# Optimization experiments

Hardware: AMD Instinct MI355X
Metric: run time of the kernel (lower is better)

## Reference

```python
import jax, jax.numpy as jnp
import numpy as np

B = 4096            # batch
D = 2048            # inp_dim
H = 16              # head_num
HD = 128            # head_dim; H*HD == D (required by residual + hidden reshape)
NB = H              # BlockLinear num_blocks = head_num
BD = HD // NB       # 8, block size inside each head vector
PROJ = int((4.0 / 3.0) * H * HD)  # 2730
EPS_LN = float(D)   # flax nn.LayerNorm(inp_dim): first positional arg is epsilon (source bug, replicated)
EPS_GN = 1e-6       # flax GroupNorm default epsilon


def setup_inputs() -> dict:
    key = jax.random.key(0)
    ks = jax.random.split(key, 12)
    s = 0.02
    rn = lambda k, shape: (jax.random.normal(k, shape) * s).astype(jnp.float32)
    return {
        'seq': jax.random.normal(ks[0], (B, D), jnp.float32),
        'c_tm1': jnp.zeros((B, H * HD), jnp.float32),
        'n_tm1': jnp.ones((B, H * HD), jnp.float32),
        'h_tm1': jnp.zeros((B, H * HD), jnp.float32),
        'm_tm1': jnp.zeros((B, H * HD), jnp.float32),
        'ln_scale': jnp.ones((D,), jnp.float32),
        'ln_bias': jnp.zeros((D,), jnp.float32),
        'W_z': rn(ks[1], (D, H * HD)), 'b_z': jnp.zeros((H * HD,), jnp.float32),
        'W_i': rn(ks[2], (D, H * HD)), 'b_i': jnp.zeros((H * HD,), jnp.float32),
        'W_f': rn(ks[3], (D, H * HD)), 'b_f': jnp.zeros((H * HD,), jnp.float32),
        'W_o': rn(ks[4], (D, H * HD)), 'b_o': jnp.zeros((H * HD,), jnp.float32),
        'R_z_w': rn(ks[5], (NB, BD, BD)), 'R_z_b': jnp.zeros((NB, BD), jnp.float32),
        'R_i_w': rn(ks[6], (NB, BD, BD)), 'R_i_b': jnp.zeros((NB, BD), jnp.float32),
        'R_f_w': rn(ks[7], (NB, BD, BD)), 'R_f_b': jnp.zeros((NB, BD), jnp.float32),
        'R_o_w': rn(ks[8], (NB, BD, BD)), 'R_o_b': jnp.zeros((NB, BD), jnp.float32),
        'gn_scale': jnp.ones((HD,), jnp.float32),
        'gn_bias': jnp.zeros((HD,), jnp.float32),
        'up_w': rn(ks[9], (H * HD, 2 * PROJ)), 'up_b': jnp.zeros((2 * PROJ,), jnp.float32),
        'down_w': rn(ks[10], (PROJ, D)), 'down_b': jnp.zeros((D,), jnp.float32),
    }


def reference(seq, c_tm1, n_tm1, h_tm1, m_tm1, ln_scale, ln_bias,
              W_z, b_z, W_i, b_i, W_f, b_f, W_o, b_o,
              R_z_w, R_z_b, R_i_w, R_i_b, R_f_w, R_f_b, R_o_w, R_o_b,
              gn_scale, gn_bias, up_w, up_b, down_w, down_b):
    Bq = seq.shape[0]
    # LayerNorm (epsilon == inp_dim, replicating the flax positional-arg quirk)
    mu = jnp.mean(seq, axis=-1, keepdims=True)
    var = jnp.mean((seq - mu) ** 2, axis=-1, keepdims=True)
    x_t = (seq - mu) / jnp.sqrt(var + EPS_LN) * ln_scale + ln_bias
    x_c = x_t  # use_conv=False path

    # Block-diagonal recurrence: h (B,H,HD) -> (B,H,NB,BD), same (BD,BD) block per head
    h_blk = h_tm1.reshape(Bq, H, NB, BD)
    def blk(w, b):
        return (jnp.einsum('bhnd,nde->bhne', h_blk, w) + b).reshape(Bq, -1)

    i_t = x_c @ W_i + b_i + blk(R_i_w, R_i_b)
    f_t = x_c @ W_f + b_f + blk(R_f_w, R_f_b)
    z_t = x_t @ W_z + b_z + blk(R_z_w, R_z_b)
    o_t = x_t @ W_o + b_o + blk(R_o_w, R_o_b)

    # max-stabilized exponential gating
    m_t = jnp.maximum(f_t + m_tm1, i_t)
    i_e = jnp.exp(i_t - m_t)
    f_e = jnp.exp(f_t - m_t + m_tm1)
    z = jnp.tanh(z_t)
    o = jax.nn.sigmoid(o_t)
    c_t = f_e * c_tm1 + i_e * z
    n_t = f_e * n_tm1 + i_e
    h_t = o * (c_t / n_t)

    # flax GroupNorm(num_groups=H) on (B, H, HD): channels=HD split into H groups,
    # reduction over the spatial head axis and each channel group, per (B, group)
    G = H
    Dg = HD // G
    x4 = h_t.reshape(Bq, H, G, Dg)
    mu2 = jnp.mean(x4, axis=(1, 3), keepdims=True)
    var2 = jnp.mean((x4 - mu2) ** 2, axis=(1, 3), keepdims=True)
    xn = ((x4 - mu2) / jnp.sqrt(var2 + EPS_GN)).reshape(Bq, H, HD)
    out = (xn * gn_scale + gn_bias).reshape(Bq, -1)

    up = out @ up_w + up_b
    out1, out2 = jnp.split(up, 2, axis=-1)
    out = (out1 + jax.nn.gelu(out2)) @ down_w + down_b
    return (out + seq, (c_t, n_t, h_t, m_t))
```

## Files before the change

kernel.cpp:

```cpp
#include <hip/hip_runtime.h>
#include <hip/hip_bf16.h>
#include <math.h>

#define BATCH 4096
#define DIM   2048
#define PROJ  2730
#define UPN   5460
#define KPAD  2816
#define NUP   5504
#define NG    8192
#define ROWF  8388608ull

typedef __attribute__((ext_vector_type(8))) short          bf16x8;
typedef __attribute__((ext_vector_type(4))) float          f32x4;
typedef __attribute__((ext_vector_type(8))) unsigned short ushort8;

__device__ __forceinline__ unsigned short f2b(float f) {
    unsigned u = __builtin_bit_cast(unsigned, f);
    u += 0x7fffu + ((u >> 16) & 1u);
    return (unsigned short)(u >> 16);
}
__device__ __forceinline__ float b2f(unsigned short h) {
    unsigned u = ((unsigned)h) << 16;
    return __builtin_bit_cast(float, u);
}

__global__ __launch_bounds__(256)
void ln_kernel(const float* __restrict__ seq, const float* __restrict__ sc,
               const float* __restrict__ bi, unsigned short* __restrict__ X)
{
    __shared__ float red[4][2];
    int b = blockIdx.x, tid = threadIdx.x;
    const float* row = seq + (size_t)b * DIM;
    float4 v0 = ((const float4*)row)[tid];
    float4 v1 = ((const float4*)row)[tid + 256];
    float s  = v0.x + v0.y + v0.z + v0.w + v1.x + v1.y + v1.z + v1.w;
    float ss = v0.x*v0.x + v0.y*v0.y + v0.z*v0.z + v0.w*v0.w
             + v1.x*v1.x + v1.y*v1.y + v1.z*v1.z + v1.w*v1.w;
    #pragma unroll
    for (int off = 32; off; off >>= 1) { s += __shfl_down(s, off); ss += __shfl_down(ss, off); }
    int wid = tid >> 6, lane = tid & 63;
    if (lane == 0) { red[wid][0] = s; red[wid][1] = ss; }
    __syncthreads();
    if (tid == 0) {
        float S = 0.f, SS = 0.f;
        #pragma unroll
        for (int w = 0; w < 4; ++w) { S += red[w][0]; SS += red[w][1]; }
        float mu  = S * (1.0f / DIM);
        float var = SS * (1.0f / DIM) - mu * mu;
        red[0][0] = mu;
        red[0][1] = rsqrtf(var + 2048.0f);
    }
    __syncthreads();
    float mu = red[0][0], r = red[0][1];
    unsigned short* xr = X + (size_t)b * DIM;
    {
        float4 s0 = ((const float4*)sc)[tid];
        float4 b0 = ((const float4*)bi)[tid];
        ushort4 o;
        o.x = f2b((v0.x - mu) * r * s0.x + b0.x);
        o.y = f2b((v0.y - mu) * r * s0.y + b0.y);
        o.z = f2b((v0.z - mu) * r * s0.z + b0.z);
        o.w = f2b((v0.w - mu) * r * s0.w + b0.w);
        ((ushort4*)xr)[tid] = o;
    }
    {
        float4 s1 = ((const float4*)sc)[tid + 256];
        float4 b1 = ((const float4*)bi)[tid + 256];
        ushort4 o;
        o.x = f2b((v1.x - mu) * r * s1.x + b1.x);
        o.y = f2b((v1.y - mu) * r * s1.y + b1.y);
        o.z = f2b((v1.z - mu) * r * s1.z + b1.z);
        o.w = f2b((v1.w - mu) * r * s1.w + b1.w);
        ((ushort4*)xr)[tid + 256] = o;
    }
}

__global__ __launch_bounds__(256)
void wt_kernel(const float* __restrict__ B0, const float* __restrict__ B1,
               const float* __restrict__ B2, const float* __restrict__ B3,
               unsigned short* __restrict__ out, int N, int ldk, int Kvalid, int Nvalid)
{
    __shared__ float lt[64][65];
    int z = blockIdx.z;
    const float* in = (z == 0) ? B0 : (z == 1) ? B1 : (z == 2) ? B2 : B3;
    unsigned short* op = out + (size_t)z * 2048u * (size_t)ldk;

    int k0 = blockIdx.x * 64, n0 = blockIdx.y * 64;
    int t = threadIdx.x;
    {
        int kr = t >> 4;
        int nc = (t & 15) * 4;
        #pragma unroll
        for (int rr = 0; rr < 4; ++rr) {
            int k = k0 + kr + rr * 16;
            float a = 0.f, bb = 0.f, c = 0.f, d = 0.f;
            if (k < Kvalid) {
                if (n0 + nc + 3 < Nvalid) {
                    float4 v = *(const float4*)(in + (size_t)k * N + n0 + nc);
                    a = v.x; bb = v.y; c = v.z; d = v.w;
                } else {
                    int n = n0 + nc;
                    if (n + 0 < Nvalid) a  = in[(size_t)k * N + n + 0];
                    if (n + 1 < Nvalid) bb = in[(size_t)k * N + n + 1];
                    if (n + 2 < Nvalid) c  = in[(size_t)k * N + n + 2];
                    if (n + 3 < Nvalid) d  = in[(size_t)k * N + n + 3];
                }
            }
            lt[kr + rr * 16][nc + 0] = a;
            lt[kr + rr * 16][nc + 1] = bb;
            lt[kr + rr * 16][nc + 2] = c;
            lt[kr + rr * 16][nc + 3] = d;
        }
    }
    __syncthreads();
    {
        int nr = t >> 4;
        int kc = (t & 15) * 4;
        #pragma unroll
        for (int rr = 0; rr < 4; ++rr) {
            int nn = nr + rr * 16;
            ushort4 o;
            o.x = f2b(lt[kc + 0][nn]);
            o.y = f2b(lt[kc + 1][nn]);
            o.z = f2b(lt[kc + 2][nn]);
            o.w = f2b(lt[kc + 3][nn]);
            *(ushort4*)(op + (size_t)(n0 + nn) * ldk + k0 + kc) = o;
        }
    }
}

template<int EPI>
__global__ __launch_bounds__(256)
void gemm_bf16(const unsigned short* __restrict__ A, const unsigned short* __restrict__ Bt,
               const float* __restrict__ bias, const float* __restrict__ resid,
               void* __restrict__ Cv, int Nvalid, int K, int ldc)
{
    __shared__ unsigned short As[128 * 64];
    __shared__ unsigned short Bs[128 * 64];

    int tid = threadIdx.x;
    int lane = tid & 63, wid = tid >> 6;
    int bm = blockIdx.y * 128, bn = blockIdx.x * 128;
    int wr = (wid >> 1) * 64, wc = (wid & 1) * 64;
    int fr = lane & 15, fk = (lane >> 4) * 8;

    const unsigned short* ga = A  + (size_t)(bm + wid * 32 + (lane >> 3)) * K + (lane & 7) * 8;
    const unsigned short* gb = Bt + (size_t)(bn + wid * 32 + (lane >> 3)) * K + (lane & 7) * 8;

    f32x4 zero = {0.f, 0.f, 0.f, 0.f};
    f32x4 acc[4][4];
    #pragma unroll
    for (int m = 0; m < 4; ++m)
        #pragma unroll
        for (int n = 0; n < 4; ++n) acc[m][n] = zero;

    for (int k0 = 0; k0 < K; k0 += 64) {
        #pragma unroll
        for (int c = 0; c < 4; ++c) {
            __builtin_amdgcn_global_load_lds(
                (const __attribute__((address_space(1))) void*)(ga + (size_t)(c * 8) * K + k0),
                (__attribute__((address_space(3))) void*)(As + (wid * 4 + c) * 512),
                16, 0, 0);
            __builtin_amdgcn_global_load_lds(
                (const __attribute__((address_space(1))) void*)(gb + (size_t)(c * 8) * K + k0),
                (__attribute__((address_space(3))) void*)(Bs + (wid * 4 + c) * 512),
                16, 0, 0);
        }
        __syncthreads();
        #pragma unroll
        for (int kk = 0; kk < 2; ++kk) {
            bf16x8 a[4], b[4];
            #pragma unroll
            for (int m = 0; m < 4; ++m)
                a[m] = *(const bf16x8*)(As + (wr + m * 16 + fr) * 64 + kk * 32 + fk);
            #pragma unroll
            for (int n = 0; n < 4; ++n)
                b[n] = *(const bf16x8*)(Bs + (wc + n * 16 + fr) * 64 + kk * 32 + fk);
            #pragma unroll
            for (int m = 0; m < 4; ++m)
                #pragma unroll
                for (int n = 0; n < 4; ++n)
                    acc[m][n] = __builtin_amdgcn_mfma_f32_16x16x32_bf16(a[m], b[n], acc[m][n], 0, 0, 0);
        }
        __syncthreads();
    }

    int row0 = bm + wr + (lane >> 4) * 4;
    int col0 = bn + wc + fr;
    #pragma unroll
    for (int m = 0; m < 4; ++m) {
        #pragma unroll
        for (int n = 0; n < 4; ++n) {
            int col = col0 + n * 16;
            #pragma unroll
            for (int r = 0; r < 4; ++r) {
                int row = row0 + m * 16 + r;
                float v = acc[m][n][r];
                if (EPI == 0) {
                    ((unsigned short*)Cv)[(size_t)row * ldc + col] = f2b(v);
                } else if (EPI == 1) {
                    if (col < Nvalid)
                        ((float*)Cv)[(size_t)row * ldc + col] = v + bias[col];
                } else {
                    ((float*)Cv)[(size_t)row * ldc + col] =
                        v + bias[col] + resid[(size_t)row * ldc + col];
                }
            }
        }
    }
}

__global__ __launch_bounds__(256)
void gate_kernel(const unsigned short* __restrict__ G,
                 const float* __restrict__ b_i, const float* __restrict__ b_f,
                 const float* __restrict__ b_z, const float* __restrict__ b_o,
                 const float* __restrict__ Riw, const float* __restrict__ Rib,
                 const float* __restrict__ Rfw, const float* __restrict__ Rfb,
                 const float* __restrict__ Rzw, const float* __restrict__ Rzb,
                 const float* __restrict__ Row_, const float* __restrict__ Rob,
                 const float* __restrict__ c_tm1, const float* __restrict__ n_tm1,
                 const float* __restrict__ h_tm1, const float* __restrict__ m_tm1,
                 float* __restrict__ out)
{
    __shared__ float Rl[4][16][68];
    int tid = threadIdx.x;
    int b = blockIdx.x;

    {
        int sg = tid >> 6;
        int sn = (tid & 63) >> 2;
        int sd = (tid & 3) << 4;
        const float* Rsrc = (sg == 0) ? Riw : (sg == 1) ? Rfw : (sg == 2) ? Rzw : Row_;
        #pragma unroll
        for (int i = 0; i < 16; ++i) Rl[sg][sn][sd + i] = Rsrc[sn * 64 + sd + i];
    }
    __syncthreads();

    size_t base  = (size_t)b * DIM + (size_t)tid * 8;
    size_t baseg = (size_t)b * NG + (size_t)tid * 8;
    int n = tid & 15;

    float h8[8];
    *(float4*)&h8[0] = *(const float4*)(h_tm1 + base);
    *(float4*)&h8[4] = *(const float4*)(h_tm1 + base + 4);

    float it[8], ft[8], zt[8], ot[8];
    {
        ushort8 gi = *(const ushort8*)(G + baseg);
        ushort8 gf = *(const ushort8*)(G + baseg + 2048);
        ushort8 gz = *(const ushort8*)(G + baseg + 4096);
        ushort8 go = *(const ushort8*)(G + baseg + 6144);
        #pragma unroll
        for (int e = 0; e < 8; ++e) {
            it[e] = b2f(gi[e]); ft[e] = b2f(gf[e]);
            zt[e] = b2f(gz[e]); ot[e] = b2f(go[e]);
        }
    }

    int j0 = tid * 8;
    #pragma unroll
    for (int e = 0; e < 8; ++e) {
        float ai = b_i[j0 + e] + Rib[n * 8 + e];
        float af = b_f[j0 + e] + Rfb[n * 8 + e];
        float az = b_z[j0 + e] + Rzb[n * 8 + e];
        float ao = b_o[j0 + e] + Rob[n * 8 + e];
        #pragma unroll
        for (int d = 0; d < 8; ++d) {
            ai = fmaf(h8[d], Rl[0][n][d * 8 + e], ai);
            af = fmaf(h8[d], Rl[1][n][d * 8 + e], af);
            az = fmaf(h8[d], Rl[2][n][d * 8 + e], az);
            ao = fmaf(h8[d], Rl[3][n][d * 8 + e], ao);
        }
        it[e] += ai; ft[e] += af; zt[e] += az; ot[e] += ao;
    }

    float c8[8], n8[8], m8[8];
    *(float4*)&c8[0] = *(const float4*)(c_tm1 + base);
    *(float4*)&c8[4] = *(const float4*)(c_tm1 + base + 4);
    *(float4*)&n8[0] = *(const float4*)(n_tm1 + base);
    *(float4*)&n8[4] = *(const float4*)(n_tm1 + base + 4);
    *(float4*)&m8[0] = *(const float4*)(m_tm1 + base);
    *(float4*)&m8[4] = *(const float4*)(m_tm1 + base + 4);

    float co[8], no[8], ho[8], mo[8];
    #pragma unroll
    for (int e = 0; e < 8; ++e) {
        float mt = fmaxf(ft[e] + m8[e], it[e]);
        float ie = expf(it[e] - mt);
        float fe = expf(ft[e] - mt + m8[e]);
        float z  = tanhf(zt[e]);
        float o  = 1.0f / (1.0f + expf(-ot[e]));
        float ct = fe * c8[e] + ie * z;
        float nt = fe * n8[e] + ie;
        co[e] = ct; no[e] = nt; ho[e] = o * (ct / nt); mo[e] = mt;
    }
    *(float4*)(out + 1 * ROWF + base)     = *(float4*)&co[0];
    *(float4*)(out + 1 * ROWF + base + 4) = *(float4*)&co[4];
    *(float4*)(out + 2 * ROWF + base)     = *(float4*)&no[0];
    *(float4*)(out + 2 * ROWF + base + 4) = *(float4*)&no[4];
    *(float4*)(out + 3 * ROWF + base)     = *(float4*)&ho[0];
    *(float4*)(out + 3 * ROWF + base + 4) = *(float4*)&ho[4];
    *(float4*)(out + 4 * ROWF + base)     = *(float4*)&mo[0];
    *(float4*)(out + 4 * ROWF + base + 4) = *(float4*)&mo[4];
}

__global__ __launch_bounds__(256)
void gn_kernel(const float* __restrict__ H_, const float* __restrict__ gs,
               const float* __restrict__ gb, unsigned short* __restrict__ X)
{
    __shared__ float sh[2048];
    __shared__ float smu[16], srs[16];
    int b = blockIdx.x, tid = threadIdx.x;
    const float* hr = H_ + (size_t)b * DIM;
    ((float4*)sh)[tid]       = ((const float4*)hr)[tid];
    ((float4*)sh)[tid + 256] = ((const float4*)hr)[tid + 256];
    __syncthreads();

    int g = tid >> 4, t = tid & 15;
    float s = 0.f, ss = 0.f;
    #pragma unroll
    for (int d = 0; d < 8; ++d) {
        float v = sh[t * 128 + g * 8 + d];
        s += v; ss += v * v;
    }
    #pragma unroll
    for (int off = 8; off; off >>= 1) {
        s  += __shfl_xor(s, off, 16);
        ss += __shfl_xor(ss, off, 16);
    }
    if (t == 0) {
        float mu  = s * (1.0f / 128.0f);
        float var = ss * (1.0f / 128.0f) - mu * mu;
        smu[g] = mu;
        srs[g] = rsqrtf(var + 1e-6f);
    }
    __syncthreads();

    int gg = tid & 15;
    float mu = smu[gg], r = srs[gg];
    unsigned short* xr = X + (size_t)b * DIM;
    ushort8 w;
    #pragma unroll
    for (int e = 0; e < 8; ++e) {
        int j  = tid * 8 + e;
        int ci = (gg << 3) + e;
        w[e] = f2b((sh[j] - mu) * r * gs[ci] + gb[ci]);
    }
    *(ushort8*)(xr + (size_t)tid * 8) = w;
}

__global__ __launch_bounds__(256)
void fuse_gelu(const float* __restrict__ U, unsigned short* __restrict__ F)
{
    int j = blockIdx.x * 256 + threadIdx.x;
    int b = blockIdx.y;
    float v = 0.f;
    if (j < PROJ) {
        const float* ur = U + (size_t)b * UPN;
        float x1 = ur[j], x2 = ur[j + PROJ];
        float inner = 0.7978845608028654f * (x2 + 0.044715f * x2 * x2 * x2);
        v = x1 + 0.5f * x2 * (1.0f + tanhf(inner));
    }
    F[(size_t)b * KPAD + j] = f2b(v);
}

extern "C" void kernel_launch(void* const* d_in, const int* in_sizes, int n_in,
                              void* d_out, int out_size, void* d_ws, size_t ws_size,
                              hipStream_t stream)
{
    const float* seq   = (const float*)d_in[0];
    const float* c_tm1 = (const float*)d_in[1];
    const float* n_tm1 = (const float*)d_in[2];
    const float* h_tm1 = (const float*)d_in[3];
    const float* m_tm1 = (const float*)d_in[4];
    const float* ln_s  = (const float*)d_in[5];
    const float* ln_b  = (const float*)d_in[6];
    const float* W_z = (const float*)d_in[7];   const float* b_z = (const float*)d_in[8];
    const float* W_i = (const float*)d_in[9];   const float* b_i = (const float*)d_in[10];
    const float* W_f = (const float*)d_in[11];  const float* b_f = (const float*)d_in[12];
    const float* W_o = (const float*)d_in[13];  const float* b_o = (const float*)d_in[14];
    const float* Rzw = (const float*)d_in[15];  const float* Rzb = (const float*)d_in[16];
    const float* Riw = (const float*)d_in[17];  const float* Rib = (const float*)d_in[18];
    const float* Rfw = (const float*)d_in[19];  const float* Rfb = (const float*)d_in[20];
    const float* Row_ = (const float*)d_in[21]; const float* Rob = (const float*)d_in[22];
    const float* gns = (const float*)d_in[23];  const float* gnb = (const float*)d_in[24];
    const float* up_w = (const float*)d_in[25]; const float* up_b = (const float*)d_in[26];
    const float* dn_w = (const float*)d_in[27]; const float* dn_b = (const float*)d_in[28];

    float* out = (float*)d_out;

    char* p = (char*)d_ws;
    unsigned short* X   = (unsigned short*)p;                 p += 16777216;
    unsigned short* G   = (unsigned short*)p;                 p += 67108864;
    float*          U   = (float*)p;                          p += 89456640;
    unsigned short* Btg = (unsigned short*)p;                 p += 33554432;
    unsigned short* Btu = (unsigned short*)p;                 p += 22544384;
    unsigned short* Btd = (unsigned short*)p;
    unsigned short* F   = G;

    {
        dim3 g1(32, 32, 4);
        wt_kernel<<<g1, 256, 0, stream>>>(W_i, W_f, W_z, W_o, Btg, 2048, 2048, 2048, 2048);
        dim3 g2(32, 86, 1);
        wt_kernel<<<g2, 256, 0, stream>>>(up_w, nullptr, nullptr, nullptr, Btu, UPN, 2048, 2048, UPN);
        dim3 g3(44, 32, 1);
        wt_kernel<<<g3, 256, 0, stream>>>(dn_w, nullptr, nullptr, nullptr, Btd, 2048, KPAD, PROJ, 2048);
    }

    ln_kernel<<<BATCH, 256, 0, stream>>>(seq, ln_s, ln_b, X);

    {
        dim3 grid(NG / 128, BATCH / 128);
        gemm_bf16<0><<<grid, 256, 0, stream>>>(X, Btg, nullptr, nullptr, G, NG, 2048, NG);
    }

    gate_kernel<<<BATCH, 256, 0, stream>>>(G, b_i, b_f, b_z, b_o,
                                           Riw, Rib, Rfw, Rfb, Rzw, Rzb, Row_, Rob,
                                           c_tm1, n_tm1, h_tm1, m_tm1, out);

    gn_kernel<<<BATCH, 256, 0, stream>>>(out + 3 * ROWF, gns, gnb, X);

    {
        dim3 grid(NUP / 128, BATCH / 128);
        gemm_bf16<1><<<grid, 256, 0, stream>>>(X, Btu, up_b, nullptr, U, UPN, 2048, UPN);
    }

    {
        dim3 grid(KPAD / 256, BATCH);
        fuse_gelu<<<grid, 256, 0, stream>>>(U, F);
    }

    {
        dim3 grid(DIM / 128, BATCH / 128);
        gemm_bf16<2><<<grid, 256, 0, stream>>>(F, Btd, dn_b, seq, out, DIM, KPAD, DIM);
    }
}
```

Baseline: 938.6 us.

## Add 256x256 pipelined GEMM, fuse GroupNorm into gate kernel, store up-proj in bf16

Adds a 256x256-tile, 512-thread GEMM that loads tiles straight from global memory into LDS with a swizzled layout. It double-buffers K tiles across eight phases with barriers and priority hints, and is used for the gate and up-projection GEMMs. GroupNorm statistics are now computed inside the gate kernel from register values, which removes the separate gn kernel and its re-read of h_t. The up-projection output is written as bf16 rather than fp32, halving its traffic, at some precision cost before GELU. The up-weight padding grows to cover 256-wide tiles.

```diff
diff --git a/kernel.cpp b/kernel.cpp
--- a/kernel.cpp
+++ b/kernel.cpp
@@ -7,7 +7,7 @@
 #define PROJ  2730
 #define UPN   5460
 #define KPAD  2816
-#define NUP   5504
+#define NUPP  5632
 #define NG    8192
 #define ROWF  8388608ull
 
@@ -131,10 +131,146 @@
 }
 
 template<int EPI>
+__global__ __launch_bounds__(512, 2)
+void gemm256(const unsigned short* __restrict__ A, const unsigned short* __restrict__ Bt,
+             const float* __restrict__ bias, void* __restrict__ Cv,
+             int Nvalid, int K, int ldc)
+{
+    __shared__ __attribute__((aligned(16))) char lds[131072];
+    const char* ldsc = (const char*)lds;
+
+    const int tid  = threadIdx.x;
+    const int lane = tid & 63, wid = tid >> 6;
+    const int wr = wid >> 2, wc = wid & 3;
+    const int fr = lane & 15, fkq = lane >> 4;
+    const int bm = blockIdx.y * 256, bn = blockIdx.x * 256;
+
+    const int r8  = lane >> 3;
+    const int swz = (lane & 7) ^ r8;
+    const unsigned short* gA = A  + (size_t)(bm + wid * 8 + r8) * K + swz * 8;
+    const unsigned short* gB = Bt + (size_t)(bn + wid * 8 + r8) * K + swz * 8;
+
+    const int cp0 = ((0 + fkq) ^ (fr & 7)) * 16;
+    const int cp1 = ((4 + fkq) ^ (fr & 7)) * 16;
+    const int aBase = wr * 16384 + fr * 128;
+    const int bBase = 65536 + (wc >> 1) * 16384 + ((wc & 1) * 64 + fr) * 128;
+
+#define GLL(gsrc, ldsoff)                                                      \
+    __builtin_amdgcn_global_load_lds(                                          \
+        (const __attribute__((address_space(1))) void*)(gsrc),                 \
+        (__attribute__((address_space(3))) void*)(lds + (ldsoff)), 16, 0, 0)
+
+#define STAGE_A(b, h, kt) do {                                                 \
+        GLL(gA + (size_t)((h) * 128 + 0) * K + (size_t)(kt) * 64,              \
+            (b) * 32768 + (h) * 16384 + (0 + wid * 8) * 128);                  \
+        GLL(gA + (size_t)((h) * 128 + 64) * K + (size_t)(kt) * 64,             \
+            (b) * 32768 + (h) * 16384 + (64 + wid * 8) * 128);                 \
+    } while (0)
+#define STAGE_B(b, h, kt) do {                                                 \
+        GLL(gB + (size_t)((h) * 128 + 0) * K + (size_t)(kt) * 64,              \
+            65536 + (b) * 32768 + (h) * 16384 + (0 + wid * 8) * 128);          \
+        GLL(gB + (size_t)((h) * 128 + 64) * K + (size_t)(kt) * 64,             \
+            65536 + (b) * 32768 + (h) * 16384 + (64 + wid * 8) * 128);         \
+    } while (0)
+
+    f32x4 acc[8][4];
+    #pragma unroll
+    for (int m = 0; m < 8; ++m)
+        #pragma unroll
+        for (int n = 0; n < 4; ++n) acc[m][n] = (f32x4){0.f, 0.f, 0.f, 0.f};
+
+    bf16x8 breg[4][2];
+    bf16x8 areg[2][2];
+
+    STAGE_B(0, 0, 0); STAGE_B(0, 1, 0);
+    STAGE_A(0, 0, 0); STAGE_A(0, 1, 0);
+    STAGE_B(1, 0, 1); STAGE_B(1, 1, 1);
+    asm volatile("s_waitcnt vmcnt(4)" ::: "memory");
+    __builtin_amdgcn_s_barrier();
+
+#define PHASE(bb, p, READB, STG, TAIL)                                         \
+    {                                                                          \
+        if (READB) {                                                           \
+            _Pragma("unroll")                                                  \
+            for (int nn = 0; nn < 4; ++nn) {                                   \
+                breg[nn][0] = *(const bf16x8*)(ldsc + (bb) * 32768 + bBase + nn * 2048 + cp0); \
+                breg[nn][1] = *(const bf16x8*)(ldsc + (bb) * 32768 + bBase + nn * 2048 + cp1); \
+            }                                                                  \
+        }                                                                      \
+        _Pragma("unroll")                                                      \
+        for (int mi = 0; mi < 2; ++mi) {                                       \
+            areg[mi][0] = *(const bf16x8*)(ldsc + (bb) * 32768 + aBase + ((p) * 2 + mi) * 2048 + cp0); \
+            areg[mi][1] = *(const bf16x8*)(ldsc + (bb) * 32768 + aBase + ((p) * 2 + mi) * 2048 + cp1); \
+        }                                                                      \
+        STG;                                                                   \
+        __builtin_amdgcn_sched_barrier(0);                                     \
+        __builtin_amdgcn_s_barrier();                                          \
+        asm volatile("s_waitcnt lgkmcnt(0)" ::: "memory");                     \
+        __builtin_amdgcn_sched_barrier(0);                                     \
+        __builtin_amdgcn_s_setprio(1);                                         \
+        _Pragma("unroll")                                                      \
+        for (int kk = 0; kk < 2; ++kk)                                         \
+            _Pragma("unroll")                                                  \
+            for (int mi = 0; mi < 2; ++mi)                                     \
+                _Pragma("unroll")                                              \
+                for (int nn = 0; nn < 4; ++nn)                                 \
+                    acc[(p) * 2 + mi][nn] = __builtin_amdgcn_mfma_f32_16x16x32_bf16( \
+                        areg[mi][kk], breg[nn][kk], acc[(p) * 2 + mi][nn], 0, 0, 0); \
+        __builtin_amdgcn_s_setprio(0);                                         \
+        TAIL;                                                                  \
+        __builtin_amdgcn_s_barrier();                                          \
+    }
+
+    const int NIT = K / 128;
+    for (int it = 0; it < NIT; ++it) {
+        const bool last = (it == NIT - 1);
+        const int T = it * 2;
+        PHASE(0, 0, 1, STAGE_A(1, 0, T + 1), ((void)0))
+        PHASE(0, 1, 0, STAGE_A(1, 1, T + 1), ((void)0))
+        PHASE(0, 2, 0, if (!last) STAGE_B(0, 0, T + 2), ((void)0))
+        PHASE(0, 3, 0, if (!last) STAGE_B(0, 1, T + 2),
+              if (last) { asm volatile("s_waitcnt vmcnt(0)" ::: "memory"); }
+              else      { asm volatile("s_waitcnt vmcnt(4)" ::: "memory"); })
+        PHASE(1, 0, 1, if (!last) STAGE_A(0, 0, T + 2), ((void)0))
+        PHASE(1, 1, 0, if (!last) STAGE_A(0, 1, T + 2), ((void)0))
+        PHASE(1, 2, 0, if (!last) STAGE_B(1, 0, T + 3), ((void)0))
+        PHASE(1, 3, 0, if (!last) STAGE_B(1, 1, T + 3),
+              if (!last) { asm volatile("s_waitcnt vmcnt(4)" ::: "memory"); })
+    }
+
+    const int q = lane >> 4;
+    const int row0 = bm + wr * 128 + q * 4;
+    const int col0 = bn + wc * 64 + fr;
+    unsigned short* C = (unsigned short*)Cv;
+    #pragma unroll
+    for (int mm = 0; mm < 8; ++mm) {
+        #pragma unroll
+        for (int nn = 0; nn < 4; ++nn) {
+            int col = col0 + nn * 16;
+            if (EPI == 0) {
+                #pragma unroll
+                for (int r = 0; r < 4; ++r)
+                    C[(size_t)(row0 + mm * 16 + r) * ldc + col] = f2b(acc[mm][nn][r]);
+            } else {
+                if (col < Nvalid) {
+                    float bv = bias[col];
+                    #pragma unroll
+                    for (int r = 0; r < 4; ++r)
+                        C[(size_t)(row0 + mm * 16 + r) * ldc + col] = f2b(acc[mm][nn][r] + bv);
+                }
+            }
+        }
+    }
+#undef PHASE
+#undef STAGE_A
+#undef STAGE_B
+#undef GLL
+}
+
 __global__ __launch_bounds__(256)
-void gemm_bf16(const unsigned short* __restrict__ A, const unsigned short* __restrict__ Bt,
-               const float* __restrict__ bias, const float* __restrict__ resid,
-               void* __restrict__ Cv, int Nvalid, int K, int ldc)
+void gemm_bf16_dn(const unsigned short* __restrict__ A, const unsigned short* __restrict__ Bt,
+                  const float* __restrict__ bias, const float* __restrict__ resid,
+                  float* __restrict__ Cv, int K, int ldc)
 {
     __shared__ unsigned short As[128 * 64];
     __shared__ unsigned short Bs[128 * 64];
@@ -196,16 +332,8 @@
             #pragma unroll
             for (int r = 0; r < 4; ++r) {
                 int row = row0 + m * 16 + r;
-                float v = acc[m][n][r];
-                if (EPI == 0) {
-                    ((unsigned short*)Cv)[(size_t)row * ldc + col] = f2b(v);
-                } else if (EPI == 1) {
-                    if (col < Nvalid)
-                        ((float*)Cv)[(size_t)row * ldc + col] = v + bias[col];
-                } else {
-                    ((float*)Cv)[(size_t)row * ldc + col] =
-                        v + bias[col] + resid[(size_t)row * ldc + col];
-                }
+                Cv[(size_t)row * ldc + col] =
+                    acc[m][n][r] + bias[col] + resid[(size_t)row * ldc + col];
             }
         }
     }
@@ -221,11 +349,14 @@
                  const float* __restrict__ Row_, const float* __restrict__ Rob,
                  const float* __restrict__ c_tm1, const float* __restrict__ n_tm1,
                  const float* __restrict__ h_tm1, const float* __restrict__ m_tm1,
-                 float* __restrict__ out)
+                 const float* __restrict__ gs, const float* __restrict__ gb,
+                 float* __restrict__ out, unsigned short* __restrict__ X)
 {
     __shared__ float Rl[4][16][68];
+    __shared__ float gp[2][4][16];
     int tid = threadIdx.x;
     int b = blockIdx.x;
+    int lane = tid & 63, wid = tid >> 6;
 
     {
         int sg = tid >> 6;
@@ -303,62 +434,35 @@
     *(float4*)(out + 3 * ROWF + base + 4) = *(float4*)&ho[4];
     *(float4*)(out + 4 * ROWF + base)     = *(float4*)&mo[0];
     *(float4*)(out + 4 * ROWF + base + 4) = *(float4*)&mo[4];
+
+    float s = 0.f, ss = 0.f;
+    #pragma unroll
+    for (int e = 0; e < 8; ++e) { s += ho[e]; ss += ho[e] * ho[e]; }
+    s += __shfl_xor(s, 16); ss += __shfl_xor(ss, 16);
+    s += __shfl_xor(s, 32); ss += __shfl_xor(ss, 32);
+    if (lane < 16) { gp[0][wid][lane] = s; gp[1][wid][lane] = ss; }
+    __syncthreads();
+    int g = tid & 15;
+    float S  = gp[0][0][g] + gp[0][1][g] + gp[0][2][g] + gp[0][3][g];
+    float SS = gp[1][0][g] + gp[1][1][g] + gp[1][2][g] + gp[1][3][g];
+    float mu = S * (1.0f / 128.0f);
+    float rs = rsqrtf(SS * (1.0f / 128.0f) - mu * mu + 1e-6f);
+    ushort8 w;
+    #pragma unroll
+    for (int e = 0; e < 8; ++e)
+        w[e] = f2b((ho[e] - mu) * rs * gs[g * 8 + e] + gb[g * 8 + e]);
+    *(ushort8*)(X + base) = w;
 }
 
 __global__ __launch_bounds__(256)
-void gn_kernel(const float* __restrict__ H_, const float* __restrict__ gs,
-               const float* __restrict__ gb, unsigned short* __restrict__ X)
-{
-    __shared__ float sh[2048];
-    __shared__ float smu[16], srs[16];
-    int b = blockIdx.x, tid = threadIdx.x;
-    const float* hr = H_ + (size_t)b * DIM;
-    ((float4*)sh)[tid]       = ((const float4*)hr)[tid];
-    ((float4*)sh)[tid + 256] = ((const float4*)hr)[tid + 256];
-    __syncthreads();
-
-    int g = tid >> 4, t = tid & 15;
-    float s = 0.f, ss = 0.f;
-    #pragma unroll
-    for (int d = 0; d < 8; ++d) {
-        float v = sh[t * 128 + g * 8 + d];
-        s += v; ss += v * v;
-    }
-    #pragma unroll
-    for (int off = 8; off; off >>= 1) {
-        s  += __shfl_xor(s, off, 16);
-        ss += __shfl_xor(ss, off, 16);
-    }
-    if (t == 0) {
-        float mu  = s * (1.0f / 128.0f);
-        float var = ss * (1.0f / 128.0f) - mu * mu;
-        smu[g] = mu;
-        srs[g] = rsqrtf(var + 1e-6f);
-    }
-    __syncthreads();
-
-    int gg = tid & 15;
-    float mu = smu[gg], r = srs[gg];
-    unsigned short* xr = X + (size_t)b * DIM;
-    ushort8 w;
-    #pragma unroll
-    for (int e = 0; e < 8; ++e) {
-        int j  = tid * 8 + e;
-        int ci = (gg << 3) + e;
-        w[e] = f2b((sh[j] - mu) * r * gs[ci] + gb[ci]);
-    }
-    *(ushort8*)(xr + (size_t)tid * 8) = w;
-}
-
-__global__ __launch_bounds__(256)
-void fuse_gelu(const float* __restrict__ U, unsigned short* __restrict__ F)
+void fuse_gelu(const unsigned short* __restrict__ U, unsigned short* __restrict__ F)
 {
     int j = blockIdx.x * 256 + threadIdx.x;
     int b = blockIdx.y;
     float v = 0.f;
     if (j < PROJ) {
-        const float* ur = U + (size_t)b * UPN;
-        float x1 = ur[j], x2 = ur[j + PROJ];
+        const unsigned short* ur = U + (size_t)b * UPN;
+        float x1 = b2f(ur[j]), x2 = b2f(ur[j + PROJ]);
         float inner = 0.7978845608028654f * (x2 + 0.044715f * x2 * x2 * x2);
         v = x1 + 0.5f * x2 * (1.0f + tanhf(inner));
     }
@@ -391,18 +495,18 @@
     float* out = (float*)d_out;
 
     char* p = (char*)d_ws;
-    unsigned short* X   = (unsigned short*)p;                 p += 16777216;
-    unsigned short* G   = (unsigned short*)p;                 p += 67108864;
-    float*          U   = (float*)p;                          p += 89456640;
-    unsigned short* Btg = (unsigned short*)p;                 p += 33554432;
-    unsigned short* Btu = (unsigned short*)p;                 p += 22544384;
+    unsigned short* X   = (unsigned short*)p;  p += 16777216;
+    unsigned short* G   = (unsigned short*)p;  p += 67108864;
+    unsigned short* U   = (unsigned short*)p;  p += 44728320;
+    unsigned short* Btg = (unsigned short*)p;  p += 33554432;
+    unsigned short* Btu = (unsigned short*)p;  p += 23068672;
     unsigned short* Btd = (unsigned short*)p;
     unsigned short* F   = G;
 
     {
         dim3 g1(32, 32, 4);
         wt_kernel<<<g1, 256, 0, stream>>>(W_i, W_f, W_z, W_o, Btg, 2048, 2048, 2048, 2048);
-        dim3 g2(32, 86, 1);
+        dim3 g2(32, 88, 1);
         wt_kernel<<<g2, 256, 0, stream>>>(up_w, nullptr, nullptr, nullptr, Btu, UPN, 2048, 2048, UPN);
         dim3 g3(44, 32, 1);
         wt_kernel<<<g3, 256, 0, stream>>>(dn_w, nullptr, nullptr, nullptr, Btd, 2048, KPAD, PROJ, 2048);
@@ -411,19 +515,17 @@
     ln_kernel<<<BATCH, 256, 0, stream>>>(seq, ln_s, ln_b, X);
 
     {
-        dim3 grid(NG / 128, BATCH / 128);
-        gemm_bf16<0><<<grid, 256, 0, stream>>>(X, Btg, nullptr, nullptr, G, NG, 2048, NG);
+        dim3 grid(NG / 256, BATCH / 256);
+        gemm256<0><<<grid, 512, 0, stream>>>(X, Btg, nullptr, G, NG, 2048, NG);
     }
 
     gate_kernel<<<BATCH, 256, 0, stream>>>(G, b_i, b_f, b_z, b_o,
                                            Riw, Rib, Rfw, Rfb, Rzw, Rzb, Row_, Rob,
-                                           c_tm1, n_tm1, h_tm1, m_tm1, out);
-
-    gn_kernel<<<BATCH, 256, 0, stream>>>(out + 3 * ROWF, gns, gnb, X);
-
-    {
-        dim3 grid(NUP / 128, BATCH / 128);
-        gemm_bf16<1><<<grid, 256, 0, stream>>>(X, Btu, up_b, nullptr, U, UPN, 2048, UPN);
+                                           c_tm1, n_tm1, h_tm1, m_tm1, gns, gnb, out, X);
+
+    {
+        dim3 grid(NUPP / 256, BATCH / 256);
+        gemm256<1><<<grid, 512, 0, stream>>>(X, Btu, up_b, U, UPN, 2048, UPN);
     }
 
     {
@@ -433,6 +535,6 @@
 
     {
         dim3 grid(DIM / 128, BATCH / 128);
-        gemm_bf16<2><<<grid, 256, 0, stream>>>(F, Btd, dn_b, seq, out, DIM, KPAD, DIM);
-    }
-}
+        gemm_bf16_dn<<<grid, 256, 0, stream>>>(F, Btd, dn_b, seq, out, KPAD, DIM);
+    }
+}
```

Measured after the change: 810.5 us. 13.6% less time.
